# Performance work log

Hardware: AMD Instinct MI355X
Metric: run time of the kernel (lower is better)

Reference implementation:

```python
import jax, jax.numpy as jnp
import numpy as np

B, N, C = 2, 50000, 256
H, W = 8, 256  # num_heads, window_size
HD = C // H


def setup_inputs() -> dict:
    key = jax.random.key(0)
    k1, k2, k3, k4, k5 = jax.random.split(key, 5)
    s = 1.0 / np.sqrt(C)
    return {
        "x": jax.random.normal(k1, (B, N, C), dtype=jnp.float32),
        "qkv_w": jax.random.uniform(k2, (C, 3 * C), jnp.float32, -s, s),
        "qkv_b": jax.random.uniform(k3, (3 * C,), jnp.float32, -s, s),
        "proj_w": jax.random.uniform(k4, (C, C), jnp.float32, -s, s),
        "proj_b": jax.random.uniform(k5, (C,), jnp.float32, -s, s),
    }


def reference(x, qkv_w, qkv_b, proj_w, proj_b):
    Bv, Nv, Cv = x.shape
    pad = (W - Nv % W) % W
    xp = jnp.pad(x, ((0, 0), (0, pad), (0, 0)))  # (B, Np, C)
    nW = (Nv + pad) // W
    xw = xp.reshape(Bv, nW, W, Cv)
    qkv = xw @ qkv_w + qkv_b                     # (B, nW, W, 3C)
    qkv = qkv.reshape(Bv, nW, W, 3, H, HD)
    q, k, v = qkv[..., 0, :, :], qkv[..., 1, :, :], qkv[..., 2, :, :]  # (B,nW,W,H,HD)
    scale = HD ** (-0.5)
    attn = jnp.einsum('bwihd,bwjhd->bwhij', q, k) * scale  # (B,nW,H,W,W)
    attn = jax.nn.softmax(attn, axis=-1)
    out = jnp.einsum('bwhij,bwjhd->bwihd', attn, v)        # (B,nW,W,H,HD)
    out = out.reshape(Bv, nW, W, Cv)
    out = out @ proj_w + proj_b
    out = out.reshape(Bv, nW * W, Cv)[:, :Nv]
    return out
```

## Files before the change

### kernel.cpp

```cpp
#include <hip/hip_runtime.h>

typedef short bf16x8 __attribute__((ext_vector_type(8)));
typedef short bf16x4 __attribute__((ext_vector_type(4)));
typedef float f32x4  __attribute__((ext_vector_type(4)));

static constexpr int Nd    = 50000;
static constexpr int Cd    = 256;
static constexpr int Hd    = 8;
static constexpr int Wd    = 256;
static constexpr int NWd   = (Nd + Wd - 1) / Wd;
static constexpr int NROWS = 2 * Nd;

#define DEV static __device__ __forceinline__

DEV short f2bf(float f) {
  unsigned u = __float_as_uint(f);
  u += 0x7fffu + ((u >> 16) & 1u);
  return (short)(u >> 16);
}

DEV bf16x8 ldfrag(const short* p) {
  bf16x4 a = *(const bf16x4*)(p);
  bf16x4 b = *(const bf16x4*)(p + 16);
  return __builtin_shufflevector(a, b, 0, 1, 2, 3, 4, 5, 6, 7);
}

DEV f32x4 mfma16(bf16x8 a, bf16x8 b, f32x4 c) {
  return __builtin_amdgcn_mfma_f32_16x16x32_bf16(a, b, c, 0, 0, 0);
}

__global__ __launch_bounds__(512, 2)
void wattn_qkv_attn(const float* __restrict__ x,
                    const float* __restrict__ qkv_w,
                    const float* __restrict__ qkv_b,
                    float* __restrict__ out)
{
  __shared__ short lds[30208];
  short (*Xs)[36]  = (short(*)[36]) (lds);
  short (*Qs)[36]  = (short(*)[36]) (lds);
  short (*Ps)[36]  = (short(*)[36]) (lds);
  short (*Wt)[36]  = (short(*)[36]) (lds + 9216);
  short (*Ks)[36]  = (short(*)[36]) (lds + 12672);
  short (*Vt)[260] = (short(*)[260])(lds + 21888);

  const int blk = blockIdx.x;
  const int b   = blk / NWd;
  const int w   = blk % NWd;
  const int n0  = w * Wd;
  const int valid = (Nd - n0 < Wd) ? (Nd - n0) : Wd;

  const float* xw = x   + ((size_t)b * Nd + n0) * Cd;
  float*       ow = out + ((size_t)b * Nd + n0) * Cd;

  const int tid  = threadIdx.x;
  const int wid  = tid >> 6;
  const int lane = tid & 63;
  const int l15  = lane & 15;
  const int l4   = lane >> 4;
  const int rb   = wid * 32;
  const float scale = 0.1767766952966369f;

  for (int h = 0; h < Hd; ++h) {
    f32x4 acc[2][6];
#pragma unroll
    for (int i = 0; i < 2; ++i)
#pragma unroll
      for (int j = 0; j < 6; ++j) acc[i][j] = (f32x4){0.f, 0.f, 0.f, 0.f};

    for (int kc = 0; kc < 8; ++kc) {
      __syncthreads();
#pragma unroll
      for (int i = 0; i < 4; ++i) {
        int idx = tid + i * 512;
        int row = idx >> 3;
        int q   = (idx & 7) * 4;
        float4 v = make_float4(0.f, 0.f, 0.f, 0.f);
        if (row < valid) v = *(const float4*)&xw[(size_t)row * Cd + kc * 32 + q];
        bf16x4 s4 = { f2bf(v.x), f2bf(v.y), f2bf(v.z), f2bf(v.w) };
        *(bf16x4*)&Xs[row][q] = s4;
      }
#pragma unroll
      for (int i = 0; i < 6; ++i) {
        int idx = tid + i * 512;
        int sec = idx >> 10;
        int k   = (idx >> 5) & 31;
        int n   = idx & 31;
        float v = qkv_w[(size_t)(kc * 32 + k) * (3 * Cd) + sec * Cd + h * 32 + n];
        Wt[sec * 32 + n][k] = f2bf(v);
      }
      __syncthreads();
      bf16x8 a0 = ldfrag(&Xs[rb + l15][l4 * 4]);
      bf16x8 a1 = ldfrag(&Xs[rb + 16 + l15][l4 * 4]);
#pragma unroll
      for (int fc = 0; fc < 6; ++fc) {
        bf16x8 bb = ldfrag(&Wt[fc * 16 + l15][l4 * 4]);
        acc[0][fc] = mfma16(a0, bb, acc[0][fc]);
        acc[1][fc] = mfma16(a1, bb, acc[1][fc]);
      }
    }

#pragma unroll
    for (int fc = 0; fc < 6; ++fc) {
      int sec  = fc >> 1;
      int colh = (fc & 1) * 16 + l15;
      float bias = qkv_b[sec * Cd + h * 32 + colh];
#pragma unroll
      for (int fr = 0; fr < 2; ++fr) {
        int row0 = rb + fr * 16 + l4 * 4;
        f32x4 v = acc[fr][fc];
        if (sec == 0) {
#pragma unroll
          for (int r = 0; r < 4; ++r) Qs[row0 + r][colh] = f2bf((v[r] + bias) * scale);
        } else if (sec == 1) {
#pragma unroll
          for (int r = 0; r < 4; ++r) Ks[row0 + r][colh] = f2bf(v[r] + bias);
        } else {
          bf16x4 s4 = { f2bf(v[0] + bias), f2bf(v[1] + bias),
                        f2bf(v[2] + bias), f2bf(v[3] + bias) };
          *(bf16x4*)&Vt[colh][row0] = s4;
        }
      }
    }
    __syncthreads();

    bf16x8 qa0 = ldfrag(&Qs[rb + l15][l4 * 4]);
    bf16x8 qa1 = ldfrag(&Qs[rb + 16 + l15][l4 * 4]);
    f32x4 s[2][16];
#pragma unroll
    for (int fc = 0; fc < 16; ++fc) {
      bf16x8 kb = ldfrag(&Ks[fc * 16 + l15][l4 * 4]);
      f32x4 z = (f32x4){0.f, 0.f, 0.f, 0.f};
      s[0][fc] = mfma16(qa0, kb, z);
      s[1][fc] = mfma16(qa1, kb, z);
    }

    float sminv[2][4];
#pragma unroll
    for (int fr = 0; fr < 2; ++fr)
#pragma unroll
      for (int r = 0; r < 4; ++r) {
        float m = -1e30f;
#pragma unroll
        for (int fc = 0; fc < 16; ++fc) m = fmaxf(m, s[fr][fc][r]);
#pragma unroll
        for (int d = 1; d < 16; d <<= 1) m = fmaxf(m, __shfl_xor(m, d));
        float t = 0.f;
#pragma unroll
        for (int fc = 0; fc < 16; ++fc) {
          float e = __expf(s[fr][fc][r] - m);
          s[fr][fc][r] = e;
          t += e;
        }
#pragma unroll
        for (int d = 1; d < 16; d <<= 1) t += __shfl_xor(t, d);
        sminv[fr][r] = 1.f / t;
      }

    f32x4 o[2][2];
    o[0][0] = o[0][1] = o[1][0] = o[1][1] = (f32x4){0.f, 0.f, 0.f, 0.f};
#pragma unroll
    for (int c = 0; c < 8; ++c) {
#pragma unroll
      for (int fr = 0; fr < 2; ++fr)
#pragma unroll
        for (int fc2 = 0; fc2 < 2; ++fc2) {
          f32x4 v = s[fr][c * 2 + fc2];
          int row0 = rb + fr * 16 + l4 * 4;
#pragma unroll
          for (int r = 0; r < 4; ++r)
            Ps[row0 + r][fc2 * 16 + l15] = f2bf(v[r]);
        }
      bf16x8 pa0 = ldfrag(&Ps[rb + l15][l4 * 4]);
      bf16x8 pa1 = ldfrag(&Ps[rb + 16 + l15][l4 * 4]);
#pragma unroll
      for (int fc2 = 0; fc2 < 2; ++fc2) {
        bf16x8 vb = ldfrag(&Vt[fc2 * 16 + l15][c * 32 + l4 * 4]);
        o[0][fc2] = mfma16(pa0, vb, o[0][fc2]);
        o[1][fc2] = mfma16(pa1, vb, o[1][fc2]);
      }
    }

#pragma unroll
    for (int fr = 0; fr < 2; ++fr)
#pragma unroll
      for (int fc2 = 0; fc2 < 2; ++fc2)
#pragma unroll
        for (int r = 0; r < 4; ++r) {
          int row = rb + fr * 16 + l4 * 4 + r;
          if (row < valid)
            ow[(size_t)row * Cd + h * 32 + fc2 * 16 + l15] = o[fr][fc2][r] * sminv[fr][r];
        }
  }
}

__global__ __launch_bounds__(512, 2)
void wattn_proj(float* data,
                const float* __restrict__ proj_w,
                const float* __restrict__ proj_b)
{
  __shared__ short Os[256][36];
  __shared__ short Wt[256][36];

  const int r0   = blockIdx.x * 256;
  const int tid  = threadIdx.x;
  const int wid  = tid >> 6;
  const int lane = tid & 63;
  const int l15  = lane & 15;
  const int l4   = lane >> 4;
  const int rb   = wid * 32;

  f32x4 acc[2][16];
#pragma unroll
  for (int i = 0; i < 2; ++i)
#pragma unroll
    for (int j = 0; j < 16; ++j) acc[i][j] = (f32x4){0.f, 0.f, 0.f, 0.f};

  for (int kc = 0; kc < 8; ++kc) {
    __syncthreads();
#pragma unroll
    for (int i = 0; i < 4; ++i) {
      int idx = tid + i * 512;
      int row = idx >> 3;
      int q   = (idx & 7) * 4;
      float4 v = make_float4(0.f, 0.f, 0.f, 0.f);
      if (r0 + row < NROWS) v = *(const float4*)&data[(size_t)(r0 + row) * Cd + kc * 32 + q];
      bf16x4 s4 = { f2bf(v.x), f2bf(v.y), f2bf(v.z), f2bf(v.w) };
      *(bf16x4*)&Os[row][q] = s4;
    }
#pragma unroll
    for (int i = 0; i < 16; ++i) {
      int idx = tid + i * 512;
      int k = idx >> 8;
      int n = idx & 255;
      Wt[n][k] = f2bf(proj_w[(size_t)(kc * 32 + k) * Cd + n]);
    }
    __syncthreads();
    bf16x8 a0 = ldfrag(&Os[rb + l15][l4 * 4]);
    bf16x8 a1 = ldfrag(&Os[rb + 16 + l15][l4 * 4]);
#pragma unroll
    for (int fc = 0; fc < 16; ++fc) {
      bf16x8 bb = ldfrag(&Wt[fc * 16 + l15][l4 * 4]);
      acc[0][fc] = mfma16(a0, bb, acc[0][fc]);
      acc[1][fc] = mfma16(a1, bb, acc[1][fc]);
    }
  }

#pragma unroll
  for (int fc = 0; fc < 16; ++fc) {
    float bias = proj_b[fc * 16 + l15];
#pragma unroll
    for (int fr = 0; fr < 2; ++fr) {
      int row0 = r0 + rb + fr * 16 + l4 * 4;
#pragma unroll
      for (int r = 0; r < 4; ++r)
        if (row0 + r < NROWS)
          data[(size_t)(row0 + r) * Cd + fc * 16 + l15] = acc[fr][fc][r] + bias;
    }
  }
}

extern "C" void kernel_launch(void* const* d_in, const int* in_sizes, int n_in,
                              void* d_out, int out_size, void* d_ws, size_t ws_size,
                              hipStream_t stream) {
  const float* x      = (const float*)d_in[0];
  const float* qkv_w  = (const float*)d_in[1];
  const float* qkv_b  = (const float*)d_in[2];
  const float* proj_w = (const float*)d_in[3];
  const float* proj_b = (const float*)d_in[4];
  float* out = (float*)d_out;

  wattn_qkv_attn<<<dim3(2 * NWd), dim3(512), 0, stream>>>(x, qkv_w, qkv_b, out);
  wattn_proj<<<dim3((NROWS + 255) / 256), dim3(512), 0, stream>>>(out, proj_w, proj_b);
}
```

Baseline: 613.3 us.

## Split attention grid per head, stage bf16 intermediate, shrink proj tiles

The attention kernel now launches one block per (head, window) instead of looping over the eight heads inside each block. This multiplies the grid by eight to fill the GPU better, and each block streams the x tile straight from global memory into registers with a one-step prefetch instead of staging it in LDS. The attention output is written as bf16 to the workspace when it is large enough, which halves the intermediate traffic. The projection kernel uses 128-row tiles and occupancy hints are raised. In exchange, each head's block re-reads the whole x window, so x is loaded eight times overall.

Result: slower. 763.1 us (+24.4%).

```diff
diff --git a/kernel.cpp b/kernel.cpp
--- a/kernel.cpp
+++ b/kernel.cpp
@@ -6,10 +6,10 @@
 
 static constexpr int Nd    = 50000;
 static constexpr int Cd    = 256;
-static constexpr int Hd    = 8;
 static constexpr int Wd    = 256;
-static constexpr int NWd   = (Nd + Wd - 1) / Wd;
-static constexpr int NROWS = 2 * Nd;
+static constexpr int NWd   = 196;
+static constexpr int NB2   = 392;
+static constexpr int NROWS = 100000;
 
 #define DEV static __device__ __forceinline__
 
@@ -29,14 +29,21 @@
   return __builtin_amdgcn_mfma_f32_16x16x32_bf16(a, b, c, 0, 0, 0);
 }
 
-__global__ __launch_bounds__(512, 2)
+DEV bf16x8 pack8(float4 lo, float4 hi) {
+  bf16x8 r;
+  r[0] = f2bf(lo.x); r[1] = f2bf(lo.y); r[2] = f2bf(lo.z); r[3] = f2bf(lo.w);
+  r[4] = f2bf(hi.x); r[5] = f2bf(hi.y); r[6] = f2bf(hi.z); r[7] = f2bf(hi.w);
+  return r;
+}
+
+__global__ __launch_bounds__(512, 4)
 void wattn_qkv_attn(const float* __restrict__ x,
                     const float* __restrict__ qkv_w,
                     const float* __restrict__ qkv_b,
-                    float* __restrict__ out)
+                    float* __restrict__ out,
+                    short* __restrict__ obf, int useWs)
 {
   __shared__ short lds[30208];
-  short (*Xs)[36]  = (short(*)[36]) (lds);
   short (*Qs)[36]  = (short(*)[36]) (lds);
   short (*Ps)[36]  = (short(*)[36]) (lds);
   short (*Wt)[36]  = (short(*)[36]) (lds + 9216);
@@ -44,13 +51,15 @@
   short (*Vt)[260] = (short(*)[260])(lds + 21888);
 
   const int blk = blockIdx.x;
-  const int b   = blk / NWd;
-  const int w   = blk % NWd;
+  const int h   = blk / NB2;
+  const int wb  = blk % NB2;
+  const int b   = wb / NWd;
+  const int w   = wb % NWd;
   const int n0  = w * Wd;
   const int valid = (Nd - n0 < Wd) ? (Nd - n0) : Wd;
 
-  const float* xw = x   + ((size_t)b * Nd + n0) * Cd;
-  float*       ow = out + ((size_t)b * Nd + n0) * Cd;
+  const float* xw = x + ((size_t)b * Nd + n0) * Cd;
+  const size_t gro = (size_t)b * Nd + n0;
 
   const int tid  = threadIdx.x;
   const int wid  = tid >> 6;
@@ -60,173 +69,172 @@
   const int rb   = wid * 32;
   const float scale = 0.1767766952966369f;
 
-  for (int h = 0; h < Hd; ++h) {
-    f32x4 acc[2][6];
-#pragma unroll
-    for (int i = 0; i < 2; ++i)
-#pragma unroll
-      for (int j = 0; j < 6; ++j) acc[i][j] = (f32x4){0.f, 0.f, 0.f, 0.f};
-
-    for (int kc = 0; kc < 8; ++kc) {
-      __syncthreads();
-#pragma unroll
-      for (int i = 0; i < 4; ++i) {
-        int idx = tid + i * 512;
-        int row = idx >> 3;
-        int q   = (idx & 7) * 4;
-        float4 v = make_float4(0.f, 0.f, 0.f, 0.f);
-        if (row < valid) v = *(const float4*)&xw[(size_t)row * Cd + kc * 32 + q];
-        bf16x4 s4 = { f2bf(v.x), f2bf(v.y), f2bf(v.z), f2bf(v.w) };
-        *(bf16x4*)&Xs[row][q] = s4;
-      }
-#pragma unroll
-      for (int i = 0; i < 6; ++i) {
-        int idx = tid + i * 512;
-        int sec = idx >> 10;
-        int k   = (idx >> 5) & 31;
-        int n   = idx & 31;
-        float v = qkv_w[(size_t)(kc * 32 + k) * (3 * Cd) + sec * Cd + h * 32 + n];
-        Wt[sec * 32 + n][k] = f2bf(v);
-      }
-      __syncthreads();
-      bf16x8 a0 = ldfrag(&Xs[rb + l15][l4 * 4]);
-      bf16x8 a1 = ldfrag(&Xs[rb + 16 + l15][l4 * 4]);
-#pragma unroll
-      for (int fc = 0; fc < 6; ++fc) {
-        bf16x8 bb = ldfrag(&Wt[fc * 16 + l15][l4 * 4]);
-        acc[0][fc] = mfma16(a0, bb, acc[0][fc]);
-        acc[1][fc] = mfma16(a1, bb, acc[1][fc]);
-      }
-    }
-
+  auto loadA = [&](int kc, int rowofs) -> bf16x8 {
+    int row = rb + rowofs + l15;
+    float4 lo = make_float4(0.f, 0.f, 0.f, 0.f), hi = lo;
+    if (row < valid) {
+      const float* p = &xw[(size_t)row * Cd + kc * 32 + l4 * 4];
+      lo = *(const float4*)p;
+      hi = *(const float4*)(p + 16);
+    }
+    return pack8(lo, hi);
+  };
+
+  f32x4 acc[2][6];
+#pragma unroll
+  for (int i = 0; i < 2; ++i)
+#pragma unroll
+    for (int j = 0; j < 6; ++j) acc[i][j] = (f32x4){0.f, 0.f, 0.f, 0.f};
+
+  bf16x8 a0 = loadA(0, 0), a1 = loadA(0, 16);
+
+  for (int kc = 0; kc < 8; ++kc) {
+    __syncthreads();
+#pragma unroll
+    for (int i = 0; i < 6; ++i) {
+      int idx = tid + i * 512;
+      int sec = idx >> 10;
+      int k   = (idx >> 5) & 31;
+      int n   = idx & 31;
+      float v = qkv_w[(size_t)(kc * 32 + k) * (3 * Cd) + sec * Cd + h * 32 + n];
+      Wt[sec * 32 + n][k] = f2bf(v);
+    }
+    bf16x8 na0 = a0, na1 = a1;
+    if (kc < 7) { na0 = loadA(kc + 1, 0); na1 = loadA(kc + 1, 16); }
+    __syncthreads();
 #pragma unroll
     for (int fc = 0; fc < 6; ++fc) {
-      int sec  = fc >> 1;
-      int colh = (fc & 1) * 16 + l15;
-      float bias = qkv_b[sec * Cd + h * 32 + colh];
-#pragma unroll
-      for (int fr = 0; fr < 2; ++fr) {
+      bf16x8 bb = ldfrag(&Wt[fc * 16 + l15][l4 * 4]);
+      acc[0][fc] = mfma16(a0, bb, acc[0][fc]);
+      acc[1][fc] = mfma16(a1, bb, acc[1][fc]);
+    }
+    a0 = na0; a1 = na1;
+  }
+
+#pragma unroll
+  for (int fc = 0; fc < 6; ++fc) {
+    int sec  = fc >> 1;
+    int colh = (fc & 1) * 16 + l15;
+    float bias = qkv_b[sec * Cd + h * 32 + colh];
+#pragma unroll
+    for (int fr = 0; fr < 2; ++fr) {
+      int row0 = rb + fr * 16 + l4 * 4;
+      f32x4 v = acc[fr][fc];
+      if (sec == 0) {
+#pragma unroll
+        for (int r = 0; r < 4; ++r) Qs[row0 + r][colh] = f2bf((v[r] + bias) * scale);
+      } else if (sec == 1) {
+#pragma unroll
+        for (int r = 0; r < 4; ++r) Ks[row0 + r][colh] = f2bf(v[r] + bias);
+      } else {
+        bf16x4 s4 = { f2bf(v[0] + bias), f2bf(v[1] + bias),
+                      f2bf(v[2] + bias), f2bf(v[3] + bias) };
+        *(bf16x4*)&Vt[colh][row0] = s4;
+      }
+    }
+  }
+  __syncthreads();
+
+  bf16x8 qa0 = ldfrag(&Qs[rb + l15][l4 * 4]);
+  bf16x8 qa1 = ldfrag(&Qs[rb + 16 + l15][l4 * 4]);
+  f32x4 s[2][16];
+#pragma unroll
+  for (int fc = 0; fc < 16; ++fc) {
+    bf16x8 kb = ldfrag(&Ks[fc * 16 + l15][l4 * 4]);
+    f32x4 z = (f32x4){0.f, 0.f, 0.f, 0.f};
+    s[0][fc] = mfma16(qa0, kb, z);
+    s[1][fc] = mfma16(qa1, kb, z);
+  }
+
+  float sminv[2][4];
+#pragma unroll
+  for (int fr = 0; fr < 2; ++fr)
+#pragma unroll
+    for (int r = 0; r < 4; ++r) {
+      float m = -1e30f;
+#pragma unroll
+      for (int fc = 0; fc < 16; ++fc) m = fmaxf(m, s[fr][fc][r]);
+#pragma unroll
+      for (int d = 1; d < 16; d <<= 1) m = fmaxf(m, __shfl_xor(m, d));
+      float t = 0.f;
+#pragma unroll
+      for (int fc = 0; fc < 16; ++fc) {
+        float e = __expf(s[fr][fc][r] - m);
+        s[fr][fc][r] = e;
+        t += e;
+      }
+#pragma unroll
+      for (int d = 1; d < 16; d <<= 1) t += __shfl_xor(t, d);
+      sminv[fr][r] = 1.f / t;
+    }
+
+  f32x4 o[2][2];
+  o[0][0] = o[0][1] = o[1][0] = o[1][1] = (f32x4){0.f, 0.f, 0.f, 0.f};
+#pragma unroll
+  for (int c = 0; c < 8; ++c) {
+#pragma unroll
+    for (int fr = 0; fr < 2; ++fr)
+#pragma unroll
+      for (int fc2 = 0; fc2 < 2; ++fc2) {
+        f32x4 v = s[fr][c * 2 + fc2];
         int row0 = rb + fr * 16 + l4 * 4;
-        f32x4 v = acc[fr][fc];
-        if (sec == 0) {
-#pragma unroll
-          for (int r = 0; r < 4; ++r) Qs[row0 + r][colh] = f2bf((v[r] + bias) * scale);
-        } else if (sec == 1) {
-#pragma unroll
-          for (int r = 0; r < 4; ++r) Ks[row0 + r][colh] = f2bf(v[r] + bias);
-        } else {
-          bf16x4 s4 = { f2bf(v[0] + bias), f2bf(v[1] + bias),
-                        f2bf(v[2] + bias), f2bf(v[3] + bias) };
-          *(bf16x4*)&Vt[colh][row0] = s4;
+#pragma unroll
+        for (int r = 0; r < 4; ++r)
+          Ps[row0 + r][fc2 * 16 + l15] = f2bf(v[r]);
+      }
+    bf16x8 pa0 = ldfrag(&Ps[rb + l15][l4 * 4]);
+    bf16x8 pa1 = ldfrag(&Ps[rb + 16 + l15][l4 * 4]);
+#pragma unroll
+    for (int fc2 = 0; fc2 < 2; ++fc2) {
+      bf16x8 vb = ldfrag(&Vt[fc2 * 16 + l15][c * 32 + l4 * 4]);
+      o[0][fc2] = mfma16(pa0, vb, o[0][fc2]);
+      o[1][fc2] = mfma16(pa1, vb, o[1][fc2]);
+    }
+  }
+
+#pragma unroll
+  for (int fr = 0; fr < 2; ++fr)
+#pragma unroll
+    for (int fc2 = 0; fc2 < 2; ++fc2)
+#pragma unroll
+      for (int r = 0; r < 4; ++r) {
+        int row = rb + fr * 16 + l4 * 4 + r;
+        if (row < valid) {
+          float v = o[fr][fc2][r] * sminv[fr][r];
+          int col = h * 32 + fc2 * 16 + l15;
+          if (useWs) obf[(gro + row) * Cd + col] = f2bf(v);
+          else       out[(gro + row) * Cd + col] = v;
         }
       }
-    }
-    __syncthreads();
-
-    bf16x8 qa0 = ldfrag(&Qs[rb + l15][l4 * 4]);
-    bf16x8 qa1 = ldfrag(&Qs[rb + 16 + l15][l4 * 4]);
-    f32x4 s[2][16];
-#pragma unroll
-    for (int fc = 0; fc < 16; ++fc) {
-      bf16x8 kb = ldfrag(&Ks[fc * 16 + l15][l4 * 4]);
-      f32x4 z = (f32x4){0.f, 0.f, 0.f, 0.f};
-      s[0][fc] = mfma16(qa0, kb, z);
-      s[1][fc] = mfma16(qa1, kb, z);
-    }
-
-    float sminv[2][4];
-#pragma unroll
-    for (int fr = 0; fr < 2; ++fr)
-#pragma unroll
-      for (int r = 0; r < 4; ++r) {
-        float m = -1e30f;
-#pragma unroll
-        for (int fc = 0; fc < 16; ++fc) m = fmaxf(m, s[fr][fc][r]);
-#pragma unroll
-        for (int d = 1; d < 16; d <<= 1) m = fmaxf(m, __shfl_xor(m, d));
-        float t = 0.f;
-#pragma unroll
-        for (int fc = 0; fc < 16; ++fc) {
-          float e = __expf(s[fr][fc][r] - m);
-          s[fr][fc][r] = e;
-          t += e;
-        }
-#pragma unroll
-        for (int d = 1; d < 16; d <<= 1) t += __shfl_xor(t, d);
-        sminv[fr][r] = 1.f / t;
-      }
-
-    f32x4 o[2][2];
-    o[0][0] = o[0][1] = o[1][0] = o[1][1] = (f32x4){0.f, 0.f, 0.f, 0.f};
-#pragma unroll
-    for (int c = 0; c < 8; ++c) {
-#pragma unroll
-      for (int fr = 0; fr < 2; ++fr)
-#pragma unroll
-        for (int fc2 = 0; fc2 < 2; ++fc2) {
-          f32x4 v = s[fr][c * 2 + fc2];
-          int row0 = rb + fr * 16 + l4 * 4;
-#pragma unroll
-          for (int r = 0; r < 4; ++r)
-            Ps[row0 + r][fc2 * 16 + l15] = f2bf(v[r]);
-        }
-      bf16x8 pa0 = ldfrag(&Ps[rb + l15][l4 * 4]);
-      bf16x8 pa1 = ldfrag(&Ps[rb + 16 + l15][l4 * 4]);
-#pragma unroll
-      for (int fc2 = 0; fc2 < 2; ++fc2) {
-        bf16x8 vb = ldfrag(&Vt[fc2 * 16 + l15][c * 32 + l4 * 4]);
-        o[0][fc2] = mfma16(pa0, vb, o[0][fc2]);
-        o[1][fc2] = mfma16(pa1, vb, o[1][fc2]);
-      }
-    }
-
-#pragma unroll
-    for (int fr = 0; fr < 2; ++fr)
-#pragma unroll
-      for (int fc2 = 0; fc2 < 2; ++fc2)
-#pragma unroll
-        for (int r = 0; r < 4; ++r) {
-          int row = rb + fr * 16 + l4 * 4 + r;
-          if (row < valid)
-            ow[(size_t)row * Cd + h * 32 + fc2 * 16 + l15] = o[fr][fc2][r] * sminv[fr][r];
-        }
-  }
-}
-
-__global__ __launch_bounds__(512, 2)
-void wattn_proj(float* data,
-                const float* __restrict__ proj_w,
-                const float* __restrict__ proj_b)
+}
+
+__global__ __launch_bounds__(512, 4)
+void wattn_proj2(const float* __restrict__ o_f32,
+                 const short* __restrict__ o_bf,
+                 const float* __restrict__ proj_w,
+                 const float* __restrict__ proj_b,
+                 float* __restrict__ out, int useWs)
 {
-  __shared__ short Os[256][36];
+  __shared__ short Os[128][36];
   __shared__ short Wt[256][36];
 
-  const int r0   = blockIdx.x * 256;
+  const int r0   = blockIdx.x * 128;
   const int tid  = threadIdx.x;
   const int wid  = tid >> 6;
   const int lane = tid & 63;
   const int l15  = lane & 15;
   const int l4   = lane >> 4;
-  const int rb   = wid * 32;
-
-  f32x4 acc[2][16];
-#pragma unroll
-  for (int i = 0; i < 2; ++i)
-#pragma unroll
-    for (int j = 0; j < 16; ++j) acc[i][j] = (f32x4){0.f, 0.f, 0.f, 0.f};
+
+  f32x4 acc[16];
+#pragma unroll
+  for (int j = 0; j < 16; ++j) acc[j] = (f32x4){0.f, 0.f, 0.f, 0.f};
+
+  const int srow = wid * 16 + (lane >> 2);
+  const int sq   = (lane & 3) * 8;
+  const int grow = r0 + srow;
 
   for (int kc = 0; kc < 8; ++kc) {
     __syncthreads();
-#pragma unroll
-    for (int i = 0; i < 4; ++i) {
-      int idx = tid + i * 512;
-      int row = idx >> 3;
-      int q   = (idx & 7) * 4;
-      float4 v = make_float4(0.f, 0.f, 0.f, 0.f);
-      if (r0 + row < NROWS) v = *(const float4*)&data[(size_t)(r0 + row) * Cd + kc * 32 + q];
-      bf16x4 s4 = { f2bf(v.x), f2bf(v.y), f2bf(v.z), f2bf(v.w) };
-      *(bf16x4*)&Os[row][q] = s4;
-    }
 #pragma unroll
     for (int i = 0; i < 16; ++i) {
       int idx = tid + i * 512;
@@ -234,14 +242,29 @@
       int n = idx & 255;
       Wt[n][k] = f2bf(proj_w[(size_t)(kc * 32 + k) * Cd + n]);
     }
-    __syncthreads();
-    bf16x8 a0 = ldfrag(&Os[rb + l15][l4 * 4]);
-    bf16x8 a1 = ldfrag(&Os[rb + 16 + l15][l4 * 4]);
+    if (useWs) {
+      bf16x8 v = {0,0,0,0,0,0,0,0};
+      if (grow < NROWS) v = *(const bf16x8*)&o_bf[(size_t)grow * Cd + kc * 32 + sq];
+      *(bf16x4*)&Os[srow][sq]     = __builtin_shufflevector(v, v, 0, 1, 2, 3);
+      *(bf16x4*)&Os[srow][sq + 4] = __builtin_shufflevector(v, v, 4, 5, 6, 7);
+    } else {
+      float4 lo = make_float4(0.f, 0.f, 0.f, 0.f), hi = lo;
+      if (grow < NROWS) {
+        const float* p = &o_f32[(size_t)grow * Cd + kc * 32 + sq];
+        lo = *(const float4*)p;
+        hi = *(const float4*)(p + 4);
+      }
+      bf16x4 s0 = { f2bf(lo.x), f2bf(lo.y), f2bf(lo.z), f2bf(lo.w) };
+      bf16x4 s1 = { f2bf(hi.x), f2bf(hi.y), f2bf(hi.z), f2bf(hi.w) };
+      *(bf16x4*)&Os[srow][sq]     = s0;
+      *(bf16x4*)&Os[srow][sq + 4] = s1;
+    }
+    __syncthreads();
+    bf16x8 a = ldfrag(&Os[wid * 16 + l15][l4 * 4]);
 #pragma unroll
     for (int fc = 0; fc < 16; ++fc) {
       bf16x8 bb = ldfrag(&Wt[fc * 16 + l15][l4 * 4]);
-      acc[0][fc] = mfma16(a0, bb, acc[0][fc]);
-      acc[1][fc] = mfma16(a1, bb, acc[1][fc]);
+      acc[fc] = mfma16(a, bb, acc[fc]);
     }
   }
 
@@ -249,12 +272,10 @@
   for (int fc = 0; fc < 16; ++fc) {
     float bias = proj_b[fc * 16 + l15];
 #pragma unroll
-    for (int fr = 0; fr < 2; ++fr) {
-      int row0 = r0 + rb + fr * 16 + l4 * 4;
-#pragma unroll
-      for (int r = 0; r < 4; ++r)
-        if (row0 + r < NROWS)
-          data[(size_t)(row0 + r) * Cd + fc * 16 + l15] = acc[fr][fc][r] + bias;
+    for (int r = 0; r < 4; ++r) {
+      int row = r0 + wid * 16 + l4 * 4 + r;
+      if (row < NROWS)
+        out[(size_t)row * Cd + fc * 16 + l15] = acc[fc][r] + bias;
     }
   }
 }
@@ -269,6 +290,10 @@
   const float* proj_b = (const float*)d_in[4];
   float* out = (float*)d_out;
 
-  wattn_qkv_attn<<<dim3(2 * NWd), dim3(512), 0, stream>>>(x, qkv_w, qkv_b, out);
-  wattn_proj<<<dim3((NROWS + 255) / 256), dim3(512), 0, stream>>>(out, proj_w, proj_b);
-}
+  const size_t oBytes = (size_t)NROWS * Cd * sizeof(short);
+  int useWs = (d_ws != nullptr && ws_size >= oBytes) ? 1 : 0;
+  short* obf = (short*)d_ws;
+
+  wattn_qkv_attn<<<dim3(8 * NB2), dim3(512), 0, stream>>>(x, qkv_w, qkv_b, out, obf, useWs);
+  wattn_proj2<<<dim3((NROWS + 127) / 128), dim3(512), 0, stream>>>(out, obf, proj_w, proj_b, out, useWs);
+}
```
